# Performance work log

Measured on AMD Instinct MI355X. Metric: run time of the kernel, lower is better.

## Reference

```python
import jax, jax.numpy as jnp
import numpy as np

N_VOX = 200000   # active input voxels
M_VOX = 100000   # active output voxels
K_VOL = 27       # 3x3x3 kernel offsets
C_IN = 32
C_OUT = 64


def setup_inputs() -> dict:
    key = jax.random.key(0)
    k1, k2, k3, k4 = jax.random.split(key, 4)
    feats = jax.random.normal(k1, (N_VOX, C_IN), dtype=jnp.float32)
    # kernel init ~ U(-std, std), std = 1/sqrt(in_channels * kernel_volume)
    std = 1.0 / np.sqrt(C_IN * K_VOL)
    kernel = jax.random.uniform(k2, (K_VOL, C_IN, C_OUT), dtype=jnp.float32,
                                minval=-std, maxval=std)
    # kernel map: for each offset k and output voxel m, an input voxel index
    in_idx = jax.random.randint(k3, (K_VOL, M_VOX), 0, N_VOX, dtype=jnp.int32)
    # occupancy mask: 1 if that (offset, output) pair exists in the kernel map
    mask = jax.random.randint(k4, (K_VOL, M_VOX), 0, 2, dtype=jnp.int32)
    return {"feats": feats, "kernel": kernel, "in_idx": in_idx, "mask": mask}


def reference(feats, kernel, in_idx, mask) -> jnp.ndarray:
    # Gather neighbor features per kernel offset: [K, M, C_in]
    gathered = feats[in_idx]
    gathered = gathered * mask[..., None].astype(feats.dtype)
    # Per-offset GEMM + scatter-add (offsets align on output voxels, so the
    # scatter-add is a sum over the K axis): [M, C_out]
    out = jnp.einsum('kmi,kio->mo', gathered, kernel)
    return out
```

## Files before the change

kernel.cpp:

```cpp
#include <hip/hip_runtime.h>

#define M_VOX   100000
#define N_VOX   200000
#define K_VOL   27
#define C_IN    32
#define C_OUT   64

#define STG0        14
#define STG1        (K_VOL - STG0)
#define BLK_THREADS 512
#define VOX_PER_BLK 128
#define BURST       7

typedef __bf16 bf16x8 __attribute__((ext_vector_type(8)));
typedef float  floatx4 __attribute__((ext_vector_type(4)));

#define FEATSB_BYTES  ((N_VOX + 1) * C_IN * 2)
#define BFRAG_OFF     FEATSB_BYTES

#define FEAT_CHUNKS   ((N_VOX + 1) * 4)
#define FEAT_BLOCKS   ((FEAT_CHUNKS + 255) / 256)
__global__ __launch_bounds__(256) void prep_all(
    const float* __restrict__ feats, const float* __restrict__ kernelw,
    __bf16* __restrict__ featsB, bf16x8* __restrict__ Bfrag)
{
    if (blockIdx.x < FEAT_BLOCKS) {
        const int c = blockIdx.x * 256 + threadIdx.x;
        if (c >= FEAT_CHUNKS) return;
        bf16x8 v;
        if (c < N_VOX * 4) {
            floatx4 f0 = *(const floatx4*)(feats + c * 8);
            floatx4 f1 = *(const floatx4*)(feats + c * 8 + 4);
#pragma unroll
            for (int j = 0; j < 4; ++j) { v[j] = (__bf16)f0[j]; v[4 + j] = (__bf16)f1[j]; }
        } else {
#pragma unroll
            for (int j = 0; j < 8; ++j) v[j] = (__bf16)0.0f;
        }
        *(bf16x8*)(featsB + c * 8) = v;
    } else {
        const int k    = blockIdx.x - FEAT_BLOCKS;
        const int tid  = threadIdx.x;
        const int tile = tid >> 6;
        const int col  = tid & 15;
        const int quad = (tid >> 4) & 3;
        const float* kp = kernelw + k * C_IN * C_OUT + quad * 8 * C_OUT + tile * 16 + col;
        bf16x8 b;
#pragma unroll
        for (int j = 0; j < 8; ++j) b[j] = (__bf16)kp[j * C_OUT];
        Bfrag[k * 256 + tid] = b;
    }
}

__global__ __launch_bounds__(BLK_THREADS) void sparse_conv_mfma(
    const __bf16* __restrict__ featsB,
    const bf16x8* __restrict__ BfragG,
    const int* __restrict__ in_idx,
    const int* __restrict__ mask,
    float* __restrict__ out)
{
    __shared__ bf16x8 ldsB[STG0 * 256];

    const int tid  = threadIdx.x;
    const int lane = tid & 63;
    const int wv   = tid >> 6;
    const int col  = lane & 15;
    const int quad = lane >> 4;

    const int m0 = blockIdx.x * VOX_PER_BLK + wv * 16;
    const bool active = (m0 < M_VOX);

#pragma unroll
    for (int i = tid; i < STG0 * 256; i += BLK_THREADS) ldsB[i] = BfragG[i];

    int mi[K_VOL];
    if (active) {
#pragma unroll
        for (int k = 0; k < K_VOL; ++k) {
            const int ix = in_idx[k * M_VOX + m0 + col];
            const int mk = mask[k * M_VOX + m0 + col];
            mi[k] = mk ? ix : N_VOX;
        }
    }
    __syncthreads();

    floatx4 acc0 = {0.f,0.f,0.f,0.f}, acc1 = {0.f,0.f,0.f,0.f};
    floatx4 acc2 = {0.f,0.f,0.f,0.f}, acc3 = {0.f,0.f,0.f,0.f};
    const bf16x8* lbase = ldsB + lane;
    const __bf16* fbase = featsB + quad * 8;

    bf16x8 A[BURST];

    if (active) {
#pragma unroll
        for (int j = 0; j < BURST; ++j)
            A[j] = *(const bf16x8*)(fbase + (size_t)mi[j] * C_IN);
#pragma unroll
        for (int j = 0; j < BURST; ++j) {
            const int k = j;
            bf16x8 b0 = lbase[k * 256 + 0 * 64];
            bf16x8 b1 = lbase[k * 256 + 1 * 64];
            bf16x8 b2 = lbase[k * 256 + 2 * 64];
            bf16x8 b3 = lbase[k * 256 + 3 * 64];
            acc0 = __builtin_amdgcn_mfma_f32_16x16x32_bf16(A[j], b0, acc0, 0, 0, 0);
            acc1 = __builtin_amdgcn_mfma_f32_16x16x32_bf16(A[j], b1, acc1, 0, 0, 0);
            acc2 = __builtin_amdgcn_mfma_f32_16x16x32_bf16(A[j], b2, acc2, 0, 0, 0);
            acc3 = __builtin_amdgcn_mfma_f32_16x16x32_bf16(A[j], b3, acc3, 0, 0, 0);
        }
#pragma unroll
        for (int j = 0; j < BURST; ++j)
            A[j] = *(const bf16x8*)(fbase + (size_t)mi[BURST + j] * C_IN);
#pragma unroll
        for (int j = 0; j < BURST; ++j) {
            const int k = BURST + j;
            bf16x8 b0 = lbase[k * 256 + 0 * 64];
            bf16x8 b1 = lbase[k * 256 + 1 * 64];
            bf16x8 b2 = lbase[k * 256 + 2 * 64];
            bf16x8 b3 = lbase[k * 256 + 3 * 64];
            acc0 = __builtin_amdgcn_mfma_f32_16x16x32_bf16(A[j], b0, acc0, 0, 0, 0);
            acc1 = __builtin_amdgcn_mfma_f32_16x16x32_bf16(A[j], b1, acc1, 0, 0, 0);
            acc2 = __builtin_amdgcn_mfma_f32_16x16x32_bf16(A[j], b2, acc2, 0, 0, 0);
            acc3 = __builtin_amdgcn_mfma_f32_16x16x32_bf16(A[j], b3, acc3, 0, 0, 0);
        }
    }

    __syncthreads();
#pragma unroll
    for (int i = tid; i < STG1 * 256; i += BLK_THREADS)
        ldsB[i] = BfragG[STG0 * 256 + i];
    __syncthreads();

    if (active) {
#pragma unroll
        for (int j = 0; j < BURST; ++j)
            A[j] = *(const bf16x8*)(fbase + (size_t)mi[STG0 + j] * C_IN);
#pragma unroll
        for (int j = 0; j < BURST; ++j) {
            const int k = j;
            bf16x8 b0 = lbase[k * 256 + 0 * 64];
            bf16x8 b1 = lbase[k * 256 + 1 * 64];
            bf16x8 b2 = lbase[k * 256 + 2 * 64];
            bf16x8 b3 = lbase[k * 256 + 3 * 64];
            acc0 = __builtin_amdgcn_mfma_f32_16x16x32_bf16(A[j], b0, acc0, 0, 0, 0);
            acc1 = __builtin_amdgcn_mfma_f32_16x16x32_bf16(A[j], b1, acc1, 0, 0, 0);
            acc2 = __builtin_amdgcn_mfma_f32_16x16x32_bf16(A[j], b2, acc2, 0, 0, 0);
            acc3 = __builtin_amdgcn_mfma_f32_16x16x32_bf16(A[j], b3, acc3, 0, 0, 0);
        }
#pragma unroll
        for (int j = 0; j < STG1 - BURST; ++j)
            A[j] = *(const bf16x8*)(fbase + (size_t)mi[STG0 + BURST + j] * C_IN);
#pragma unroll
        for (int j = 0; j < STG1 - BURST; ++j) {
            const int k = BURST + j;
            bf16x8 b0 = lbase[k * 256 + 0 * 64];
            bf16x8 b1 = lbase[k * 256 + 1 * 64];
            bf16x8 b2 = lbase[k * 256 + 2 * 64];
            bf16x8 b3 = lbase[k * 256 + 3 * 64];
            acc0 = __builtin_amdgcn_mfma_f32_16x16x32_bf16(A[j], b0, acc0, 0, 0, 0);
            acc1 = __builtin_amdgcn_mfma_f32_16x16x32_bf16(A[j], b1, acc1, 0, 0, 0);
            acc2 = __builtin_amdgcn_mfma_f32_16x16x32_bf16(A[j], b2, acc2, 0, 0, 0);
            acc3 = __builtin_amdgcn_mfma_f32_16x16x32_bf16(A[j], b3, acc3, 0, 0, 0);
        }

        float* op = out + (size_t)(m0 + quad * 4) * C_OUT + col;
#pragma unroll
        for (int r = 0; r < 4; ++r) {
            op[r * C_OUT + 0]  = acc0[r];
            op[r * C_OUT + 16] = acc1[r];
            op[r * C_OUT + 32] = acc2[r];
            op[r * C_OUT + 48] = acc3[r];
        }
    }
}

extern "C" void kernel_launch(void* const* d_in, const int* in_sizes, int n_in,
                              void* d_out, int out_size, void* d_ws, size_t ws_size,
                              hipStream_t stream) {
    const float* feats   = (const float*)d_in[0];
    const float* kernelw = (const float*)d_in[1];
    const int*   in_idx  = (const int*)d_in[2];
    const int*   maskp   = (const int*)d_in[3];
    float*       out     = (float*)d_out;

    __bf16* featsB = (__bf16*)d_ws;
    bf16x8* BfragP = (bf16x8*)((char*)d_ws + BFRAG_OFF);

    prep_all<<<dim3(FEAT_BLOCKS + K_VOL), dim3(256), 0, stream>>>(
        feats, kernelw, featsB, BfragP);

    const int blocks = (M_VOX + VOX_PER_BLK - 1) / VOX_PER_BLK;
    sparse_conv_mfma<<<dim3(blocks), dim3(BLK_THREADS), 0, stream>>>(
        featsB, BfragP, in_idx, maskp, out);
}
```

Baseline: 121.8 us.

## Fuse prep and conv into one cooperative persistent kernel with grid sync

```diff
diff --git a/kernel.cpp b/kernel.cpp
--- a/kernel.cpp
+++ b/kernel.cpp
@@ -1,4 +1,7 @@
 #include <hip/hip_runtime.h>
+#include <hip/hip_cooperative_groups.h>
+
+namespace cg = cooperative_groups;
 
 #define M_VOX   100000
 #define N_VOX   200000
@@ -12,14 +15,185 @@
 #define VOX_PER_BLK 128
 #define BURST       7
 
+#define TILES        ((M_VOX + VOX_PER_BLK - 1) / VOX_PER_BLK)
+#define GRID_BLOCKS  256
+#define GRID_THREADS (GRID_BLOCKS * BLK_THREADS)
+
 typedef __bf16 bf16x8 __attribute__((ext_vector_type(8)));
 typedef float  floatx4 __attribute__((ext_vector_type(4)));
 
 #define FEATSB_BYTES  ((N_VOX + 1) * C_IN * 2)
 #define BFRAG_OFF     FEATSB_BYTES
-
 #define FEAT_CHUNKS   ((N_VOX + 1) * 4)
 #define FEAT_BLOCKS   ((FEAT_CHUNKS + 255) / 256)
+
+__device__ __forceinline__ void conv_tile(
+    const int tileIdx,
+    const __bf16* __restrict__ featsB,
+    const bf16x8* __restrict__ BfragG,
+    const int*    __restrict__ in_idx,
+    const int*    __restrict__ mask,
+    float*        __restrict__ out,
+    bf16x8* ldsB)
+{
+    const int tid  = threadIdx.x;
+    const int lane = tid & 63;
+    const int wv   = tid >> 6;
+    const int col  = lane & 15;
+    const int quad = lane >> 4;
+
+    const int m0 = tileIdx * VOX_PER_BLK + wv * 16;
+    const bool active = (m0 < M_VOX);
+
+#pragma unroll
+    for (int i = tid; i < STG0 * 256; i += BLK_THREADS) ldsB[i] = BfragG[i];
+
+    int mi[K_VOL];
+    if (active) {
+#pragma unroll
+        for (int k = 0; k < K_VOL; ++k) {
+            const int ix = in_idx[k * M_VOX + m0 + col];
+            const int mk = mask[k * M_VOX + m0 + col];
+            mi[k] = mk ? ix : N_VOX;
+        }
+    }
+    __syncthreads();
+
+    floatx4 acc0 = {0.f,0.f,0.f,0.f}, acc1 = {0.f,0.f,0.f,0.f};
+    floatx4 acc2 = {0.f,0.f,0.f,0.f}, acc3 = {0.f,0.f,0.f,0.f};
+    const bf16x8* lbase = ldsB + lane;
+    const __bf16* fbase = featsB + quad * 8;
+
+    bf16x8 A[BURST];
+
+    if (active) {
+#pragma unroll
+        for (int j = 0; j < BURST; ++j)
+            A[j] = *(const bf16x8*)(fbase + (size_t)mi[j] * C_IN);
+#pragma unroll
+        for (int j = 0; j < BURST; ++j) {
+            const int k = j;
+            bf16x8 b0 = lbase[k * 256 + 0 * 64];
+            bf16x8 b1 = lbase[k * 256 + 1 * 64];
+            bf16x8 b2 = lbase[k * 256 + 2 * 64];
+            bf16x8 b3 = lbase[k * 256 + 3 * 64];
+            acc0 = __builtin_amdgcn_mfma_f32_16x16x32_bf16(A[j], b0, acc0, 0, 0, 0);
+            acc1 = __builtin_amdgcn_mfma_f32_16x16x32_bf16(A[j], b1, acc1, 0, 0, 0);
+            acc2 = __builtin_amdgcn_mfma_f32_16x16x32_bf16(A[j], b2, acc2, 0, 0, 0);
+            acc3 = __builtin_amdgcn_mfma_f32_16x16x32_bf16(A[j], b3, acc3, 0, 0, 0);
+        }
+#pragma unroll
+        for (int j = 0; j < BURST; ++j)
+            A[j] = *(const bf16x8*)(fbase + (size_t)mi[BURST + j] * C_IN);
+#pragma unroll
+        for (int j = 0; j < BURST; ++j) {
+            const int k = BURST + j;
+            bf16x8 b0 = lbase[k * 256 + 0 * 64];
+            bf16x8 b1 = lbase[k * 256 + 1 * 64];
+            bf16x8 b2 = lbase[k * 256 + 2 * 64];
+            bf16x8 b3 = lbase[k * 256 + 3 * 64];
+            acc0 = __builtin_amdgcn_mfma_f32_16x16x32_bf16(A[j], b0, acc0, 0, 0, 0);
+            acc1 = __builtin_amdgcn_mfma_f32_16x16x32_bf16(A[j], b1, acc1, 0, 0, 0);
+            acc2 = __builtin_amdgcn_mfma_f32_16x16x32_bf16(A[j], b2, acc2, 0, 0, 0);
+            acc3 = __builtin_amdgcn_mfma_f32_16x16x32_bf16(A[j], b3, acc3, 0, 0, 0);
+        }
+    }
+
+    __syncthreads();
+#pragma unroll
+    for (int i = tid; i < STG1 * 256; i += BLK_THREADS)
+        ldsB[i] = BfragG[STG0 * 256 + i];
+    __syncthreads();
+
+    if (active) {
+#pragma unroll
+        for (int j = 0; j < BURST; ++j)
+            A[j] = *(const bf16x8*)(fbase + (size_t)mi[STG0 + j] * C_IN);
+#pragma unroll
+        for (int j = 0; j < BURST; ++j) {
+            const int k = j;
+            bf16x8 b0 = lbase[k * 256 + 0 * 64];
+            bf16x8 b1 = lbase[k * 256 + 1 * 64];
+            bf16x8 b2 = lbase[k * 256 + 2 * 64];
+            bf16x8 b3 = lbase[k * 256 + 3 * 64];
+            acc0 = __builtin_amdgcn_mfma_f32_16x16x32_bf16(A[j], b0, acc0, 0, 0, 0);
+            acc1 = __builtin_amdgcn_mfma_f32_16x16x32_bf16(A[j], b1, acc1, 0, 0, 0);
+            acc2 = __builtin_amdgcn_mfma_f32_16x16x32_bf16(A[j], b2, acc2, 0, 0, 0);
+            acc3 = __builtin_amdgcn_mfma_f32_16x16x32_bf16(A[j], b3, acc3, 0, 0, 0);
+        }
+#pragma unroll
+        for (int j = 0; j < STG1 - BURST; ++j)
+            A[j] = *(const bf16x8*)(fbase + (size_t)mi[STG0 + BURST + j] * C_IN);
+#pragma unroll
+        for (int j = 0; j < STG1 - BURST; ++j) {
+            const int k = BURST + j;
+            bf16x8 b0 = lbase[k * 256 + 0 * 64];
+            bf16x8 b1 = lbase[k * 256 + 1 * 64];
+            bf16x8 b2 = lbase[k * 256 + 2 * 64];
+            bf16x8 b3 = lbase[k * 256 + 3 * 64];
+            acc0 = __builtin_amdgcn_mfma_f32_16x16x32_bf16(A[j], b0, acc0, 0, 0, 0);
+            acc1 = __builtin_amdgcn_mfma_f32_16x16x32_bf16(A[j], b1, acc1, 0, 0, 0);
+            acc2 = __builtin_amdgcn_mfma_f32_16x16x32_bf16(A[j], b2, acc2, 0, 0, 0);
+            acc3 = __builtin_amdgcn_mfma_f32_16x16x32_bf16(A[j], b3, acc3, 0, 0, 0);
+        }
+
+        float* op = out + (size_t)(m0 + quad * 4) * C_OUT + col;
+#pragma unroll
+        for (int r = 0; r < 4; ++r) {
+            op[r * C_OUT + 0]  = acc0[r];
+            op[r * C_OUT + 16] = acc1[r];
+            op[r * C_OUT + 32] = acc2[r];
+            op[r * C_OUT + 48] = acc3[r];
+        }
+    }
+}
+
+__global__ __launch_bounds__(BLK_THREADS, 4) void fused_all(
+    const float* __restrict__ feats, const float* __restrict__ kernelw,
+    const int*   __restrict__ in_idx, const int* __restrict__ mask,
+    __bf16* __restrict__ featsB, bf16x8* __restrict__ BfragG,
+    float*  __restrict__ out)
+{
+    __shared__ bf16x8 ldsB[STG0 * 256];
+
+    const int tid  = threadIdx.x;
+    const int gtid = blockIdx.x * BLK_THREADS + tid;
+
+    if (gtid < K_VOL * 256) {
+        const int k    = gtid >> 8;
+        const int t8   = gtid & 255;
+        const int tile = t8 >> 6;
+        const int col  = t8 & 15;
+        const int quad = (t8 >> 4) & 3;
+        const float* kp = kernelw + k * C_IN * C_OUT + quad * 8 * C_OUT + tile * 16 + col;
+        bf16x8 b;
+#pragma unroll
+        for (int j = 0; j < 8; ++j) b[j] = (__bf16)kp[j * C_OUT];
+        BfragG[gtid] = b;
+    }
+
+    for (int c = gtid; c < FEAT_CHUNKS; c += GRID_THREADS) {
+        bf16x8 v;
+        if (c < N_VOX * 4) {
+            floatx4 f0 = *(const floatx4*)(feats + (size_t)c * 8);
+            floatx4 f1 = *(const floatx4*)(feats + (size_t)c * 8 + 4);
+#pragma unroll
+            for (int j = 0; j < 4; ++j) { v[j] = (__bf16)f0[j]; v[4 + j] = (__bf16)f1[j]; }
+        } else {
+#pragma unroll
+            for (int j = 0; j < 8; ++j) v[j] = (__bf16)0.0f;
+        }
+        *(bf16x8*)(featsB + (size_t)c * 8) = v;
+    }
+
+    cg::this_grid().sync();
+
+    for (int t = blockIdx.x; t < TILES; t += GRID_BLOCKS) {
+        conv_tile(t, featsB, BfragG, in_idx, mask, out, ldsB);
+        __syncthreads();
+    }
+}
+
 __global__ __launch_bounds__(256) void prep_all(
     const float* __restrict__ feats, const float* __restrict__ kernelw,
     __bf16* __restrict__ featsB, bf16x8* __restrict__ Bfrag)
@@ -29,15 +203,15 @@
         if (c >= FEAT_CHUNKS) return;
         bf16x8 v;
         if (c < N_VOX * 4) {
-            floatx4 f0 = *(const floatx4*)(feats + c * 8);
-            floatx4 f1 = *(const floatx4*)(feats + c * 8 + 4);
+            floatx4 f0 = *(const floatx4*)(feats + (size_t)c * 8);
+            floatx4 f1 = *(const floatx4*)(feats + (size_t)c * 8 + 4);
 #pragma unroll
             for (int j = 0; j < 4; ++j) { v[j] = (__bf16)f0[j]; v[4 + j] = (__bf16)f1[j]; }
         } else {
 #pragma unroll
             for (int j = 0; j < 8; ++j) v[j] = (__bf16)0.0f;
         }
-        *(bf16x8*)(featsB + c * 8) = v;
+        *(bf16x8*)(featsB + (size_t)c * 8) = v;
     } else {
         const int k    = blockIdx.x - FEAT_BLOCKS;
         const int tid  = threadIdx.x;
@@ -52,7 +226,7 @@
     }
 }
 
-__global__ __launch_bounds__(BLK_THREADS) void sparse_conv_mfma(
+__global__ __launch_bounds__(BLK_THREADS) void conv_only(
     const __bf16* __restrict__ featsB,
     const bf16x8* __restrict__ BfragG,
     const int* __restrict__ in_idx,
@@ -60,117 +234,7 @@
     float* __restrict__ out)
 {
     __shared__ bf16x8 ldsB[STG0 * 256];
-
-    const int tid  = threadIdx.x;
-    const int lane = tid & 63;
-    const int wv   = tid >> 6;
-    const int col  = lane & 15;
-    const int quad = lane >> 4;
-
-    const int m0 = blockIdx.x * VOX_PER_BLK + wv * 16;
-    const bool active = (m0 < M_VOX);
-
-#pragma unroll
-    for (int i = tid; i < STG0 * 256; i += BLK_THREADS) ldsB[i] = BfragG[i];
-
-    int mi[K_VOL];
-    if (active) {
-#pragma unroll
-        for (int k = 0; k < K_VOL; ++k) {
-            const int ix = in_idx[k * M_VOX + m0 + col];
-            const int mk = mask[k * M_VOX + m0 + col];
-            mi[k] = mk ? ix : N_VOX;
-        }
-    }
-    __syncthreads();
-
-    floatx4 acc0 = {0.f,0.f,0.f,0.f}, acc1 = {0.f,0.f,0.f,0.f};
-    floatx4 acc2 = {0.f,0.f,0.f,0.f}, acc3 = {0.f,0.f,0.f,0.f};
-    const bf16x8* lbase = ldsB + lane;
-    const __bf16* fbase = featsB + quad * 8;
-
-    bf16x8 A[BURST];
-
-    if (active) {
-#pragma unroll
-        for (int j = 0; j < BURST; ++j)
-            A[j] = *(const bf16x8*)(fbase + (size_t)mi[j] * C_IN);
-#pragma unroll
-        for (int j = 0; j < BURST; ++j) {
-            const int k = j;
-            bf16x8 b0 = lbase[k * 256 + 0 * 64];
-            bf16x8 b1 = lbase[k * 256 + 1 * 64];
-            bf16x8 b2 = lbase[k * 256 + 2 * 64];
-            bf16x8 b3 = lbase[k * 256 + 3 * 64];
-            acc0 = __builtin_amdgcn_mfma_f32_16x16x32_bf16(A[j], b0, acc0, 0, 0, 0);
-            acc1 = __builtin_amdgcn_mfma_f32_16x16x32_bf16(A[j], b1, acc1, 0, 0, 0);
-            acc2 = __builtin_amdgcn_mfma_f32_16x16x32_bf16(A[j], b2, acc2, 0, 0, 0);
-            acc3 = __builtin_amdgcn_mfma_f32_16x16x32_bf16(A[j], b3, acc3, 0, 0, 0);
-        }
-#pragma unroll
-        for (int j = 0; j < BURST; ++j)
-            A[j] = *(const bf16x8*)(fbase + (size_t)mi[BURST + j] * C_IN);
-#pragma unroll
-        for (int j = 0; j < BURST; ++j) {
-            const int k = BURST + j;
-            bf16x8 b0 = lbase[k * 256 + 0 * 64];
-            bf16x8 b1 = lbase[k * 256 + 1 * 64];
-            bf16x8 b2 = lbase[k * 256 + 2 * 64];
-            bf16x8 b3 = lbase[k * 256 + 3 * 64];
-            acc0 = __builtin_amdgcn_mfma_f32_16x16x32_bf16(A[j], b0, acc0, 0, 0, 0);
-            acc1 = __builtin_amdgcn_mfma_f32_16x16x32_bf16(A[j], b1, acc1, 0, 0, 0);
-            acc2 = __builtin_amdgcn_mfma_f32_16x16x32_bf16(A[j], b2, acc2, 0, 0, 0);
-            acc3 = __builtin_amdgcn_mfma_f32_16x16x32_bf16(A[j], b3, acc3, 0, 0, 0);
-        }
-    }
-
-    __syncthreads();
-#pragma unroll
-    for (int i = tid; i < STG1 * 256; i += BLK_THREADS)
-        ldsB[i] = BfragG[STG0 * 256 + i];
-    __syncthreads();
-
-    if (active) {
-#pragma unroll
-        for (int j = 0; j < BURST; ++j)
-            A[j] = *(const bf16x8*)(fbase + (size_t)mi[STG0 + j] * C_IN);
-#pragma unroll
-        for (int j = 0; j < BURST; ++j) {
-            const int k = j;
-            bf16x8 b0 = lbase[k * 256 + 0 * 64];
-            bf16x8 b1 = lbase[k * 256 + 1 * 64];
-            bf16x8 b2 = lbase[k * 256 + 2 * 64];
-            bf16x8 b3 = lbase[k * 256 + 3 * 64];
-            acc0 = __builtin_amdgcn_mfma_f32_16x16x32_bf16(A[j], b0, acc0, 0, 0, 0);
-            acc1 = __builtin_amdgcn_mfma_f32_16x16x32_bf16(A[j], b1, acc1, 0, 0, 0);
-            acc2 = __builtin_amdgcn_mfma_f32_16x16x32_bf16(A[j], b2, acc2, 0, 0, 0);
-            acc3 = __builtin_amdgcn_mfma_f32_16x16x32_bf16(A[j], b3, acc3, 0, 0, 0);
-        }
-#pragma unroll
-        for (int j = 0; j < STG1 - BURST; ++j)
-            A[j] = *(const bf16x8*)(fbase + (size_t)mi[STG0 + BURST + j] * C_IN);
-#pragma unroll
-        for (int j = 0; j < STG1 - BURST; ++j) {
-            const int k = BURST + j;
-            bf16x8 b0 = lbase[k * 256 + 0 * 64];
-            bf16x8 b1 = lbase[k * 256 + 1 * 64];
-            bf16x8 b2 = lbase[k * 256 + 2 * 64];
-            bf16x8 b3 = lbase[k * 256 + 3 * 64];
-            acc0 = __builtin_amdgcn_mfma_f32_16x16x32_bf16(A[j], b0, acc0, 0, 0, 0);
-            acc1 = __builtin_amdgcn_mfma_f32_16x16x32_bf16(A[j], b1, acc1, 0, 0, 0);
-            acc2 = __builtin_amdgcn_mfma_f32_16x16x32_bf16(A[j], b2, acc2, 0, 0, 0);
-            acc3 = __builtin_amdgcn_mfma_f32_16x16x32_bf16(A[j], b3, acc3, 0, 0, 0);
-        }
-
-        float* op = out + (size_t)(m0 + quad * 4) * C_OUT + col;
-#pragma unroll
-        for (int r = 0; r < 4; ++r) {
-            op[r * C_OUT + 0]  = acc0[r];
-            op[r * C_OUT + 16] = acc1[r];
-            op[r * C_OUT + 32] = acc2[r];
-            op[r * C_OUT + 48] = acc3[r];
-        }
-    }
+    conv_tile(blockIdx.x, featsB, BfragG, in_idx, mask, out, ldsB);
 }
 
 extern "C" void kernel_launch(void* const* d_in, const int* in_sizes, int n_in,
@@ -185,10 +249,15 @@
     __bf16* featsB = (__bf16*)d_ws;
     bf16x8* BfragP = (bf16x8*)((char*)d_ws + BFRAG_OFF);
 
-    prep_all<<<dim3(FEAT_BLOCKS + K_VOL), dim3(256), 0, stream>>>(
-        feats, kernelw, featsB, BfragP);
-
-    const int blocks = (M_VOX + VOX_PER_BLK - 1) / VOX_PER_BLK;
-    sparse_conv_mfma<<<dim3(blocks), dim3(BLK_THREADS), 0, stream>>>(
-        featsB, BfragP, in_idx, maskp, out);
-}
+    void* args[] = { (void*)&feats, (void*)&kernelw, (void*)&in_idx, (void*)&maskp,
+                     (void*)&featsB, (void*)&BfragP, (void*)&out };
+    hipError_t e = hipLaunchCooperativeKernel((void*)fused_all, dim3(GRID_BLOCKS),
+                                              dim3(BLK_THREADS), args, 0, stream);
+    if (e != hipSuccess) {
+        prep_all<<<dim3(FEAT_BLOCKS + K_VOL), dim3(256), 0, stream>>>(
+            feats, kernelw, featsB, BfragP);
+        sparse_conv_fallback:
+        conv_only<<<dim3(TILES), dim3(BLK_THREADS), 0, stream>>>(
+            featsB, BfragP, in_idx, maskp, out);
+    }
+}
```

Result: slower. 184.3 us (+51.3%).
